# Kernel optimization log

Hardware: AMD Instinct MI355X
Metric: run time of the kernel (lower is better)

The kernel has to match this reference:

```python
import jax, jax.numpy as jnp
import numpy as np

N_NODES = 100000
N_EDGES = 1600000
D_IN = 64
D_HID = 64


def setup_inputs() -> dict:
    key = jax.random.key(0)
    ks = jax.random.split(key, 8)
    x = jax.random.normal(ks[0], (N_NODES, D_IN), dtype=jnp.float32)
    edge_index = jax.random.randint(ks[1], (2, N_EDGES), 0, N_NODES, dtype=jnp.int32)
    def glorot(k, fan_in, fan_out):
        s = jnp.sqrt(6.0 / (fan_in + fan_out)).astype(jnp.float32)
        return jax.random.uniform(k, (fan_in, fan_out), jnp.float32, -s, s)
    return {
        "x": x,
        "edge_index": edge_index,
        "W1": glorot(ks[2], D_IN, D_HID), "b1": jnp.zeros((D_HID,), jnp.float32),
        "W2": glorot(ks[3], D_HID, D_HID), "b2": jnp.zeros((D_HID,), jnp.float32),
        "W3": glorot(ks[4], D_HID, D_HID), "b3": jnp.zeros((D_HID,), jnp.float32),
    }


def _gcn_norm(edge_index, n_nodes):
    # add self-loops (as in PyG GCNConv default)
    loop = jnp.arange(n_nodes, dtype=edge_index.dtype)
    src = jnp.concatenate([edge_index[0], loop])
    dst = jnp.concatenate([edge_index[1], loop])
    deg = jax.ops.segment_sum(jnp.ones_like(dst, dtype=jnp.float32), dst,
                              num_segments=n_nodes)
    dinv = jnp.where(deg > 0, jax.lax.rsqrt(deg), 0.0)
    norm = dinv[src] * dinv[dst]  # [E + N]
    return src, dst, norm


def _gcn_conv(x, W, b, src, dst, norm, n_nodes):
    h = x @ W                      # [N, D] small GEMM
    msg = h[src] * norm[:, None]   # gather + scale  (memory-bound)
    out = jax.ops.segment_sum(msg, dst, num_segments=n_nodes)  # scatter-add
    return out + b


def reference(x, edge_index, W1, b1, W2, b2, W3, b3):
    n = x.shape[0]
    src, dst, norm = _gcn_norm(edge_index, n)
    h = jax.nn.relu(_gcn_conv(x, W1, b1, src, dst, norm, n))
    h = jax.nn.relu(_gcn_conv(h, W2, b2, src, dst, norm, n))
    return _gcn_conv(h, W3, b3, src, dst, norm, n)
```

## Files before the change

kernel.cpp:

```cpp
#include <hip/hip_runtime.h>
#include <hip/hip_bf16.h>

constexpr int NN  = 100000;
constexpr int NE  = 1600000;
constexpr int D   = 64;
constexpr int CAP = 64;

constexpr int NPB_SHIFT = 8;
constexpr int NBUK = (NN + 255) >> 8;
constexpr int BCAP = 4608;
constexpr int EPT  = 16;

typedef unsigned short ushort_t;
typedef unsigned int uint_t;
using short8 = __attribute__((ext_vector_type(8))) short;
using f32x4  = __attribute__((ext_vector_type(4))) float;

__device__ inline ushort_t f2bf(float f) {
    uint_t u = __float_as_uint(f);
    uint_t r = u + 0x7fffu + ((u >> 16) & 1u);
    return (ushort_t)(r >> 16);
}
__device__ inline float bflo(uint_t u) { return __uint_as_float(u << 16); }
__device__ inline float bfhi(uint_t u) { return __uint_as_float(u & 0xffff0000u); }
__device__ inline uint_t pkbf(float a, float b) {
    return (uint_t)f2bf(a) | ((uint_t)f2bf(b) << 16);
}

__global__ void k_zero(int* __restrict__ p, int n) {
    int i = blockIdx.x * blockDim.x + threadIdx.x;
    if (i < n) p[i] = 0;
}

__global__ void __launch_bounds__(256)
k_part(const int* __restrict__ src, const int* __restrict__ dst,
       int* __restrict__ bcur, uint_t* __restrict__ ebuf, int e) {
    __shared__ int hist[NBUK];
    __shared__ int base[NBUK];
    int t = threadIdx.x;
    for (int i = t; i < NBUK; i += 256) hist[i] = 0;
    __syncthreads();
    int start = blockIdx.x * (256 * EPT);
    uint_t pk[EPT];
    int bk[EPT];
#pragma unroll
    for (int i = 0; i < EPT; ++i) {
        int idx = start + i * 256 + t;
        if (idx < e) {
            int d = dst[idx];
            int b = d >> NPB_SHIFT;
            bk[i] = b;
            pk[i] = (uint_t)src[idx] | ((uint_t)(d & 255) << 17);
            atomicAdd(&hist[b], 1);
        } else bk[i] = -1;
    }
    __syncthreads();
    for (int i = t; i < NBUK; i += 256) {
        int c = hist[i];
        base[i] = (c > 0) ? atomicAdd(&bcur[i], c) : 0;
        hist[i] = 0;
    }
    __syncthreads();
#pragma unroll
    for (int i = 0; i < EPT; ++i) {
        if (bk[i] >= 0) {
            int b = bk[i];
            int r = atomicAdd(&hist[b], 1);
            int pos = base[b] + r;
            if (pos < BCAP) ebuf[(size_t)b * BCAP + pos] = pk[i];
        }
    }
}

__global__ void __launch_bounds__(256)
k_fill2(const uint_t* __restrict__ ebuf, const int* __restrict__ bcnt,
        int* __restrict__ deg, int* __restrict__ col, float* __restrict__ dinv,
        const float* __restrict__ x, ushort_t* __restrict__ xbf,
        const float* __restrict__ W1, const float* __restrict__ W2,
        const float* __restrict__ W3, ushort_t* __restrict__ wfrag) {
    int t = threadIdx.x;
    if (blockIdx.x >= NBUK) {
        int wi = blockIdx.x - NBUK;
        const float* W = (wi == 0) ? W1 : (wi == 1) ? W2 : W3;
        ushort_t* o = wfrag + wi * 4096;
        int l = t & 63;
#pragma unroll
        for (int it = 0; it < 2; ++it) {
            int f = (t >> 6) + it * 4;
            int kt = f >> 2, nt = f & 3;
            uint_t u[4];
#pragma unroll
            for (int i = 0; i < 4; ++i) {
                float a = W[(kt * 32 + (l >> 4) * 8 + 2 * i)     * 64 + nt * 16 + (l & 15)];
                float b = W[(kt * 32 + (l >> 4) * 8 + 2 * i + 1) * 64 + nt * 16 + (l & 15)];
                u[i] = pkbf(a, b);
            }
            *(uint4*)&o[(size_t)(f * 64 + l) * 8] = make_uint4(u[0], u[1], u[2], u[3]);
        }
        return;
    }
    __shared__ int cnt[256];
    __shared__ float sdv[256];
    int b = blockIdx.x;
    int n = min(bcnt[b], BCAP);
    int nbase = b << NPB_SHIFT;
    cnt[t] = 0;
    __syncthreads();
    for (int i = t; i < n; i += 256) {
        uint_t e = ebuf[(size_t)b * BCAP + i];
        int s = (int)(e & 0x1FFFFu);
        int d = (int)(e >> 17);
        int slot = atomicAdd(&cnt[d], 1);
        if (slot < CAP) col[(size_t)(nbase + d) * CAP + slot] = s;
    }
    __syncthreads();
    int nrow = min(256, NN - nbase);
    if (t < nrow) {
        int dgv = cnt[t];
        deg[nbase + t] = dgv;
        float dv = rsqrtf((float)(dgv + 1));
        dinv[nbase + t] = dv;
        sdv[t] = dv;
    }
    __syncthreads();
    for (int i = t; i < nrow * 16; i += 256) {
        int nl = i >> 4;
        float dv = sdv[nl];
        float4 v = ((const float4*)x)[(size_t)(nbase + nl) * 16 + (i & 15)];
        ((uint2*)xbf)[(size_t)(nbase + nl) * 16 + (i & 15)] =
            make_uint2(pkbf(v.x * dv, v.y * dv), pkbf(v.z * dv, v.w * dv));
    }
}

#define ACC8(u) do { \
    a0 += bflo((u).x); a1 += bfhi((u).x); a2 += bflo((u).y); a3 += bfhi((u).y); \
    a4 += bflo((u).z); a5 += bfhi((u).z); a6 += bflo((u).w); a7 += bfhi((u).w); } while (0)

#define GCHUNK(ck, base) do {                                               \
    int cntv = min(dg - (base), 16);                                        \
    int jj = 0;                                                             \
    for (; jj + 4 <= cntv; jj += 4) {                                       \
        int sA = __shfl((ck), c16 + jj + g2);                               \
        int sB = __shfl((ck), c16 + jj + 2 + g2);                           \
        uint4 uA = x4[(size_t)sA * 8 + q];                                  \
        uint4 uB = x4[(size_t)sB * 8 + q];                                  \
        ACC8(uA); ACC8(uB);                                                 \
    }                                                                       \
    for (; jj + 2 <= cntv; jj += 2) {                                       \
        int s = __shfl((ck), c16 + jj + g2);                                \
        uint4 u = x4[(size_t)s * 8 + q];                                    \
        ACC8(u);                                                            \
    }                                                                       \
    if (jj < cntv) {                                                        \
        int s = __shfl((ck), c16 + jj);                                     \
        uint4 u = x4[(size_t)s * 8 + q];                                    \
        if (g2) { u.x = 0u; u.y = 0u; u.z = 0u; u.w = 0u; }                 \
        ACC8(u);                                                            \
    }                                                                       \
} while (0)

template <bool RELU, bool BF16OUT>
__global__ void __launch_bounds__(256, 6)
k_layer(const ushort_t* __restrict__ xin, const int* __restrict__ col,
        const int* __restrict__ deg, const float* __restrict__ dinv,
        const ushort_t* __restrict__ wfrag, const float* __restrict__ bias,
        void* __restrict__ outv) {
    __shared__ ushort_t rowbuf[16 * D];
    __shared__ float sdv[16];
    int t = threadIdx.x, wave = t >> 6, lane = t & 63;

    short8 wfA = *(const short8*)&wfrag[(size_t)(wave * 64 + lane) * 8];
    short8 wfB = *(const short8*)&wfrag[(size_t)((4 + wave) * 64 + lane) * 8];
    float bv = bias[wave * 16 + (lane & 15)];

    int node0 = blockIdx.x * 16;
    int chain = lane >> 4;
    int c16 = lane & 48;
    int l16 = lane & 15;
    int g2  = (lane >> 3) & 1;
    int q   = lane & 7;
    const uint4* __restrict__ x4 = (const uint4*)xin;

    int n = wave * 4 + chain;
    int node = node0 + n;
    int dg = min(deg[node], CAP);
    float dv = dinv[node];
    if (l16 == 0) sdv[n] = dv;

    const int* crow = &col[(size_t)node * CAP];
    int ck0 = (l16 < dg) ? crow[l16] : 0;
    int ck1 = (16 + l16 < dg) ? crow[16 + l16] : 0;
    int ck2 = (32 + l16 < dg) ? crow[32 + l16] : 0;
    int ck3 = (48 + l16 < dg) ? crow[48 + l16] : 0;
    float a0=0.f,a1=0.f,a2=0.f,a3=0.f,a4=0.f,a5=0.f,a6=0.f,a7=0.f;
    GCHUNK(ck0, 0);
    if (dg > 16) {
        GCHUNK(ck1, 16);
        if (dg > 32) {
            GCHUNK(ck2, 32);
            if (dg > 48) GCHUNK(ck3, 48);
        }
    }
    a0 += __shfl_xor(a0, 8); a1 += __shfl_xor(a1, 8);
    a2 += __shfl_xor(a2, 8); a3 += __shfl_xor(a3, 8);
    a4 += __shfl_xor(a4, 8); a5 += __shfl_xor(a5, 8);
    a6 += __shfl_xor(a6, 8); a7 += __shfl_xor(a7, 8);
    if (l16 < 8) {
        uint4 u = x4[(size_t)node * 8 + l16];
        a0 += bflo(u.x); a1 += bfhi(u.x); a2 += bflo(u.y); a3 += bfhi(u.y);
        a4 += bflo(u.z); a5 += bfhi(u.z); a6 += bflo(u.w); a7 += bfhi(u.w);
        uint4 p = make_uint4(pkbf(a0 * dv, a1 * dv), pkbf(a2 * dv, a3 * dv),
                             pkbf(a4 * dv, a5 * dv), pkbf(a6 * dv, a7 * dv));
        ((uint4*)rowbuf)[n * 8 + (l16 ^ (n & 7))] = p;
    }
    __syncthreads();

    int arow = lane & 15, akg = lane >> 4;
    short8 af0 = *(const short8*)&rowbuf[(size_t)arow * D + (((0 * 4 + akg) ^ (arow & 7)) * 8)];
    short8 af1 = *(const short8*)&rowbuf[(size_t)arow * D + (((4 + akg) ^ (arow & 7)) * 8)];

    f32x4 c = {bv, bv, bv, bv};
    c = __builtin_amdgcn_mfma_f32_16x16x32_bf16(af0, wfA, c, 0, 0, 0);
    c = __builtin_amdgcn_mfma_f32_16x16x32_bf16(af1, wfB, c, 0, 0, 0);

    int ccol = lane & 15, crow0 = (lane >> 4) * 4;
#pragma unroll
    for (int r = 0; r < 4; ++r) {
        int row = node0 + crow0 + r;
        float o = c[r];
        if (RELU) o = fmaxf(o, 0.f);
        if (BF16OUT) {
            float dvr = sdv[crow0 + r];
            ((ushort_t*)outv)[(size_t)row * D + wave * 16 + ccol] = f2bf(o * dvr);
        } else {
            ((float*)outv)[(size_t)row * D + wave * 16 + ccol] = o;
        }
    }
}


extern "C" void kernel_launch(void* const* d_in, const int* in_sizes, int n_in,
                              void* d_out, int out_size, void* d_ws, size_t ws_size,
                              hipStream_t stream) {
    const float* x   = (const float*)d_in[0];
    const int*   ei  = (const int*)d_in[1];
    const float* W1  = (const float*)d_in[2];
    const float* b1  = (const float*)d_in[3];
    const float* W2  = (const float*)d_in[4];
    const float* b2  = (const float*)d_in[5];
    const float* W3  = (const float*)d_in[6];
    const float* b3  = (const float*)d_in[7];
    const int* src = ei;
    const int* dst = ei + NE;
    float* out = (float*)d_out;

    int* col = (int*)d_ws;
    char* p1 = (char*)(col + (size_t)NN * CAP);
    ushort_t* xbf = (ushort_t*)p1;
    char* p2 = p1 + (size_t)NN * D * 2;
    uint_t*   ebuf = (uint_t*)p2;
    ushort_t* hbf  = (ushort_t*)p2;
    int*   deg   = (int*)(p2 + (size_t)NN * D * 2);
    int*   bcur  = deg + NN;
    float* dinv  = (float*)(deg + NN + 512);
    ushort_t* wfrag = (ushort_t*)(dinv + NN);

    k_zero<<<(NBUK + 255) / 256, 256, 0, stream>>>(bcur, NBUK);

    k_part<<<(NE + 256 * EPT - 1) / (256 * EPT), 256, 0, stream>>>(src, dst, bcur, ebuf, NE);
    k_fill2<<<NBUK + 3, 256, 0, stream>>>(ebuf, bcur, deg, col, dinv, x, xbf,
                                          W1, W2, W3, wfrag);

    int layerBlocks = NN / 16;
    k_layer<true,  true ><<<layerBlocks, 256, 0, stream>>>(xbf, col, deg, dinv, wfrag,        b1, hbf);
    k_layer<true,  true ><<<layerBlocks, 256, 0, stream>>>(hbf, col, deg, dinv, wfrag + 4096, b2, xbf);
    k_layer<false, false><<<layerBlocks, 256, 0, stream>>>(xbf, col, deg, dinv, wfrag + 8192, b3, out);
}
```

Before: 151.7 us.

## Restructure neighbor gather into 8-edge groups and raise occupancy bound

Replaces the chunked gather macro with a uniform loop that loads four neighbor rows per iteration (8 edges per 16-lane chain across the two half-groups), plus one masked tail group. The weight fragment and bias loads are moved after the aggregation barrier to shorten register live ranges, and launch bounds go from 6 to 8 blocks per SIMD-level occupancy target. The intent is more memory-level parallelism per wave and higher occupancy for the latency-bound gather. The cost is that the tail group always issues four loads, and the tighter register budget may cause spills.

```diff
diff --git a/kernel.cpp b/kernel.cpp
--- a/kernel.cpp
+++ b/kernel.cpp
@@ -136,31 +136,8 @@
     a0 += bflo((u).x); a1 += bfhi((u).x); a2 += bflo((u).y); a3 += bfhi((u).y); \
     a4 += bflo((u).z); a5 += bfhi((u).z); a6 += bflo((u).w); a7 += bfhi((u).w); } while (0)
 
-#define GCHUNK(ck, base) do {                                               \
-    int cntv = min(dg - (base), 16);                                        \
-    int jj = 0;                                                             \
-    for (; jj + 4 <= cntv; jj += 4) {                                       \
-        int sA = __shfl((ck), c16 + jj + g2);                               \
-        int sB = __shfl((ck), c16 + jj + 2 + g2);                           \
-        uint4 uA = x4[(size_t)sA * 8 + q];                                  \
-        uint4 uB = x4[(size_t)sB * 8 + q];                                  \
-        ACC8(uA); ACC8(uB);                                                 \
-    }                                                                       \
-    for (; jj + 2 <= cntv; jj += 2) {                                       \
-        int s = __shfl((ck), c16 + jj + g2);                                \
-        uint4 u = x4[(size_t)s * 8 + q];                                    \
-        ACC8(u);                                                            \
-    }                                                                       \
-    if (jj < cntv) {                                                        \
-        int s = __shfl((ck), c16 + jj);                                     \
-        uint4 u = x4[(size_t)s * 8 + q];                                    \
-        if (g2) { u.x = 0u; u.y = 0u; u.z = 0u; u.w = 0u; }                 \
-        ACC8(u);                                                            \
-    }                                                                       \
-} while (0)
-
 template <bool RELU, bool BF16OUT>
-__global__ void __launch_bounds__(256, 6)
+__global__ void __launch_bounds__(256, 8)
 k_layer(const ushort_t* __restrict__ xin, const int* __restrict__ col,
         const int* __restrict__ deg, const float* __restrict__ dinv,
         const ushort_t* __restrict__ wfrag, const float* __restrict__ bias,
@@ -169,10 +146,6 @@
     __shared__ float sdv[16];
     int t = threadIdx.x, wave = t >> 6, lane = t & 63;
 
-    short8 wfA = *(const short8*)&wfrag[(size_t)(wave * 64 + lane) * 8];
-    short8 wfB = *(const short8*)&wfrag[(size_t)((4 + wave) * 64 + lane) * 8];
-    float bv = bias[wave * 16 + (lane & 15)];
-
     int node0 = blockIdx.x * 16;
     int chain = lane >> 4;
     int c16 = lane & 48;
@@ -193,13 +166,42 @@
     int ck2 = (32 + l16 < dg) ? crow[32 + l16] : 0;
     int ck3 = (48 + l16 < dg) ? crow[48 + l16] : 0;
     float a0=0.f,a1=0.f,a2=0.f,a3=0.f,a4=0.f,a5=0.f,a6=0.f,a7=0.f;
-    GCHUNK(ck0, 0);
-    if (dg > 16) {
-        GCHUNK(ck1, 16);
-        if (dg > 32) {
-            GCHUNK(ck2, 32);
-            if (dg > 48) GCHUNK(ck3, 48);
-        }
+
+    int Gf = dg >> 3;
+    for (int g = 0; g < Gf; ++g) {
+        int cc = (g < 2) ? ((g < 1) ? ck0 : ck0) : (g < 4) ? ck1 : (g < 6) ? ck2 : ck3;
+        if (g == 1) cc = ck0;
+        int lb = c16 + ((g & 1) << 3) + g2;
+        int s0 = __shfl(cc, lb);
+        int s1 = __shfl(cc, lb + 2);
+        int s2 = __shfl(cc, lb + 4);
+        int s3 = __shfl(cc, lb + 6);
+        uint4 u0 = x4[(size_t)s0 * 8 + q];
+        uint4 u1 = x4[(size_t)s1 * 8 + q];
+        uint4 u2 = x4[(size_t)s2 * 8 + q];
+        uint4 u3 = x4[(size_t)s3 * 8 + q];
+        ACC8(u0); ACC8(u1); ACC8(u2); ACC8(u3);
+    }
+    int rem = dg & 7;
+    if (rem) {
+        int g = Gf;
+        int cc = (g < 2) ? ck0 : (g < 4) ? ck1 : (g < 6) ? ck2 : ck3;
+        int lb = c16 + ((g & 1) << 3) + g2;
+        int i0 = (g << 3) + g2;
+        int s0 = __shfl(cc, lb);
+        int s1 = __shfl(cc, lb + 2);
+        int s2 = __shfl(cc, lb + 4);
+        int s3 = __shfl(cc, lb + 6);
+        uint4 u0 = x4[(size_t)s0 * 8 + q];
+        uint4 u1 = x4[(size_t)s1 * 8 + q];
+        uint4 u2 = x4[(size_t)s2 * 8 + q];
+        uint4 u3 = x4[(size_t)s3 * 8 + q];
+        uint4 z = make_uint4(0u, 0u, 0u, 0u);
+        if (i0 >= dg)     u0 = z;
+        if (i0 + 2 >= dg) u1 = z;
+        if (i0 + 4 >= dg) u2 = z;
+        if (i0 + 6 >= dg) u3 = z;
+        ACC8(u0); ACC8(u1); ACC8(u2); ACC8(u3);
     }
     a0 += __shfl_xor(a0, 8); a1 += __shfl_xor(a1, 8);
     a2 += __shfl_xor(a2, 8); a3 += __shfl_xor(a3, 8);
@@ -214,6 +216,10 @@
         ((uint4*)rowbuf)[n * 8 + (l16 ^ (n & 7))] = p;
     }
     __syncthreads();
+
+    short8 wfA = *(const short8*)&wfrag[(size_t)(wave * 64 + lane) * 8];
+    short8 wfB = *(const short8*)&wfrag[(size_t)((4 + wave) * 64 + lane) * 8];
+    float bv = bias[wave * 16 + (lane & 15)];
 
     int arow = lane & 15, akg = lane >> 4;
     short8 af0 = *(const short8*)&rowbuf[(size_t)arow * D + (((0 * 4 + akg) ^ (arow & 7)) * 8)];
```

Result: faster. 138.9 us (-8.5%).
